# Kernel tuning notes

Measured on AMD Instinct MI355X. Metric: run time of the kernel, lower is better.

The kernel has to match this reference:

```python
import jax, jax.numpy as jnp
import numpy as np

PATCH = [2, 4, 8, 16]   # square window sizes, one per head group
LAYERS = 2
C = 128                 # channel = d_input = hidden
DK = C // len(PATCH)    # 32 channels per head group


def leaky(z):
    return jax.nn.leaky_relu(z, negative_slope=0.2)


def conv2d(x, w, b, dil=1, pad=1):
    # x: (N,C,H,W), w: (O,I,3,3)
    y = jax.lax.conv_general_dilated(
        x, w, window_strides=(1, 1), padding=((pad, pad), (pad, pad)),
        rhs_dilation=(dil, dil), dimension_numbers=('NCHW', 'OIHW', 'NCHW'))
    return y + b[None, :, None, None]


def window_attn(q, k, v, bsz, ph, pw):
    # q/k/v: (b*t, dk, h, w) -> attention over t*oh*ow patch tokens of dim dk*ph*pw
    bt, dk, h, w = q.shape
    t = bt // bsz
    oh, ow = h // ph, w // pw

    def to_tok(z):
        z = z.reshape(bsz, t, dk, oh, ph, ow, pw)
        z = z.transpose(0, 1, 3, 5, 2, 4, 6)  # (b, t, oh, ow, dk, ph, pw)
        return z.reshape(bsz, t * oh * ow, dk * ph * pw)

    qt, kt, vt = to_tok(q), to_tok(k), to_tok(v)
    scale = 1.0 / jnp.sqrt(jnp.asarray(qt.shape[-1], qt.dtype))
    scores = jnp.einsum('bld,bmd->blm', qt, kt) * scale
    p = jax.nn.softmax(scores, axis=-1)
    y = jnp.einsum('blm,bmd->bld', p, vt)
    y = y.reshape(bsz, t, oh, ow, dk, ph, pw).transpose(0, 1, 4, 2, 5, 3, 6)
    return y.reshape(bt, dk, h, w)


def transformer_block(x, Wq, bq, Wk, bk, Wv, bv, Wo, bo, Wf1, bf1, Wf2, bf2, bsz):
    # 1x1 conv embeddings as channel matmuls
    q = jnp.einsum('bihw,oi->bohw', x, Wq) + bq[None, :, None, None]
    k = jnp.einsum('bihw,oi->bohw', x, Wk) + bk[None, :, None, None]
    v = jnp.einsum('bihw,oi->bohw', x, Wv) + bv[None, :, None, None]
    outs = []
    for g, p in enumerate(PATCH):
        sl = slice(g * DK, (g + 1) * DK)
        outs.append(window_attn(q[:, sl], k[:, sl], v[:, sl], bsz, p, p))
    att = jnp.concatenate(outs, axis=1)
    x = x + leaky(conv2d(att, Wo, bo, dil=1, pad=1))
    f = leaky(conv2d(x, Wf1, bf1, dil=2, pad=2))
    f = leaky(conv2d(f, Wf2, bf2, dil=1, pad=1))
    return x + f


def setup_inputs() -> dict:
    key = jax.random.key(0)
    ks = jax.random.split(key, 14)
    g = 0.02  # init gain matching init_weights normal(0, 0.02)
    x = jax.random.normal(ks[0], (8, C, 64, 64), dtype=jnp.float32)
    mk = lambda k, shape: (g * jax.random.normal(k, shape)).astype(jnp.float32)
    return {
        'x': x,
        'Wq': mk(ks[1], (LAYERS, C, C)), 'bq': jnp.zeros((LAYERS, C), jnp.float32),
        'Wk': mk(ks[2], (LAYERS, C, C)), 'bk': jnp.zeros((LAYERS, C), jnp.float32),
        'Wv': mk(ks[3], (LAYERS, C, C)), 'bv': jnp.zeros((LAYERS, C), jnp.float32),
        'Wo': mk(ks[4], (LAYERS, C, C, 3, 3)), 'bo': jnp.zeros((LAYERS, C), jnp.float32),
        'Wf1': mk(ks[5], (LAYERS, C, C, 3, 3)), 'bf1': jnp.zeros((LAYERS, C), jnp.float32),
        'Wf2': mk(ks[6], (LAYERS, C, C, 3, 3)), 'bf2': jnp.zeros((LAYERS, C), jnp.float32),
        'bsz': 2,
    }


def reference(x, Wq, bq, Wk, bk, Wv, bv, Wo, bo, Wf1, bf1, Wf2, bf2, bsz):
    for i in range(LAYERS):
        x = transformer_block(x, Wq[i], bq[i], Wk[i], bk[i], Wv[i], bv[i],
                              Wo[i], bo[i], Wf1[i], bf1[i], Wf2[i], bf2[i], bsz)
    return x
```

## Files before the change

kernel.cpp:

```cpp
#include <hip/hip_runtime.h>

__device__ __forceinline__ unsigned short f2bf(float f) {
  union { float f; unsigned int i; } c; c.f = f;
  unsigned int i = c.i;
  i += 0x7fffu + ((i >> 16) & 1u);
  return (unsigned short)(i >> 16);
}

typedef __attribute__((ext_vector_type(8))) short bf16x8;
typedef __attribute__((ext_vector_type(4))) float f32x4;


__global__ __launch_bounds__(256) void x2hwc(const float* __restrict__ X,
                                             unsigned short* __restrict__ Xh) {
  int pixg = blockIdx.x * 256 + threadIdx.x;
  int c0 = blockIdx.y * 8;
  int bt = pixg >> 12, pix = pixg & 4095;
  const float* src = X + ((size_t)bt << 19) + (size_t)c0 * 4096 + pix;
  unsigned int pk[4];
#pragma unroll
  for (int j = 0; j < 4; j++) {
    unsigned short u0 = f2bf(src[(2 * j) * 4096]);
    unsigned short u1 = f2bf(src[(2 * j + 1) * 4096]);
    pk[j] = (unsigned int)u0 | ((unsigned int)u1 << 16);
  }
  *(uint4*)(Xh + (size_t)pixg * 128 + c0) = make_uint4(pk[0], pk[1], pk[2], pk[3]);
}

__global__ __launch_bounds__(256) void wprep3(
    const float* __restrict__ s0, const float* __restrict__ s1,
    const float* __restrict__ s2, unsigned short* __restrict__ d0,
    unsigned short* __restrict__ d1, unsigned short* __restrict__ d2) {
  int idx = blockIdx.x * 256 + threadIdx.x;
  const float* s = blockIdx.y == 0 ? s0 : (blockIdx.y == 1 ? s1 : s2);
  unsigned short* d = blockIdx.y == 0 ? d0 : (blockIdx.y == 1 ? d1 : d2);
  int j = idx & 7;
  int lane = (idx >> 3) & 63;
  int kg = lane >> 4, ml = lane & 15;
  int f = idx >> 9;
  int mf = f & 3, wm = (f >> 2) & 1, cs = (f >> 3) & 3, tap = f >> 5;
  int o = wm * 64 + mf * 16 + ml;
  int i = cs * 32 + kg * 8 + j;
  d[idx] = f2bf(s[(size_t)(o * 128 + i) * 9 + tap]);
}

__global__ __launch_bounds__(256) void wprep1(
    const float* __restrict__ s0, const float* __restrict__ s1,
    const float* __restrict__ s2, unsigned short* __restrict__ d0,
    unsigned short* __restrict__ d1, unsigned short* __restrict__ d2) {
  int idx = blockIdx.x * 256 + threadIdx.x;
  const float* s = blockIdx.y == 0 ? s0 : (blockIdx.y == 1 ? s1 : s2);
  unsigned short* d = blockIdx.y == 0 ? d0 : (blockIdx.y == 1 ? d1 : d2);
  d[idx] = f2bf(s[idx]);
}

template <int MODE>
__global__ __launch_bounds__(256) void qkv_pack(
    const unsigned short* __restrict__ Xh, const unsigned short* __restrict__ Wb,
    const float* __restrict__ Bi, unsigned short* __restrict__ P,
    unsigned short* __restrict__ VtP, unsigned short* __restrict__ Ff) {
  int tid = threadIdx.x, lane = tid & 63, wid = tid >> 6;
  int wm = wid & 1, wn = wid >> 1;
  int ml = lane & 15, kg = lane >> 4;
  int m_base = blockIdx.y * 64 + wm * 32;
  int n_base = blockIdx.x * 64 + wn * 32;
  f32x4 acc[2][2];
#pragma unroll
  for (int i = 0; i < 2; i++)
#pragma unroll
    for (int j = 0; j < 2; j++) acc[i][j] = {0.f, 0.f, 0.f, 0.f};
#pragma unroll
  for (int kc = 0; kc < 128; kc += 32) {
    bf16x8 af[2], bfr[2];
#pragma unroll
    for (int mf = 0; mf < 2; mf++)
      af[mf] = *(const bf16x8*)(Wb + (size_t)(m_base + mf * 16 + ml) * 128 + kc + kg * 8);
#pragma unroll
    for (int nf = 0; nf < 2; nf++)
      bfr[nf] = *(const bf16x8*)(Xh + (size_t)(n_base + nf * 16 + ml) * 128 + kc + kg * 8);
#pragma unroll
    for (int mf = 0; mf < 2; mf++)
#pragma unroll
      for (int nf = 0; nf < 2; nf++)
        acc[mf][nf] = __builtin_amdgcn_mfma_f32_16x16x32_bf16(af[mf], bfr[nf], acc[mf][nf], 0, 0, 0);
  }
#pragma unroll
  for (int mf = 0; mf < 2; mf++)
#pragma unroll
    for (int nf = 0; nf < 2; nf++)
#pragma unroll
      for (int r = 0; r < 4; r++) {
        int c = m_base + mf * 16 + kg * 4 + r;
        int pixg = n_base + nf * 16 + ml;
        float val = acc[mf][nf][r] + Bi[c];
        int bt = pixg >> 12, pix = pixg & 4095;
        int h = pix >> 6, w = pix & 63;
        int g = c >> 5, sh = g + 1, msk = (1 << sh) - 1, ohn = 64 >> sh;
        int b = bt >> 2, t_i = bt & 3;
        int l = (t_i * ohn + (h >> sh)) * ohn + (w >> sh);
        int Dg = 32 << (2 * sh);
        int d = ((c & 31) << (2 * sh)) + ((h & msk) << sh) + (w & msk);
        if (MODE == 0) val *= rsqrtf((float)Dg);
        unsigned short bv = f2bf(val);
        size_t bofs = (size_t)b << 19;
        if (g == 0) {
          if (MODE == 0) {
            int qt = l >> 4, mlq = l & 15, cc = d >> 5, kgq = (d >> 3) & 3, j = d & 7;
            Ff[bofs + ((size_t)(qt * 4 + cc) << 9) + (kgq * 16 + mlq) * 8 + j] = bv;
          } else if (MODE == 1) {
            int ck = l >> 6, mfk = (l >> 4) & 3, mlk = l & 15;
            int cc = d >> 5, kgk = (d >> 3) & 3, j = d & 7;
            Ff[bofs + ((size_t)(ck * 16 + cc * 4 + mfk) << 9) + (kgk * 16 + mlk) * 8 + j] = bv;
          } else {
            int ck = l >> 6, part = (l >> 5) & 1, kgv = (l >> 3) & 3, j = l & 7;
            int nf = d >> 4, mlv = d & 15;
            Ff[bofs + ((size_t)(ck * 16 + nf * 2 + part) << 9) + (kgv * 16 + mlv) * 8 + j] = bv;
          }
        } else {
          size_t base = ((size_t)g << 20) + bofs;
          if (MODE != 2) {
            P[base + (size_t)l * Dg + d] = bv;
          } else {
            int Lg = 16384 >> (2 * sh);
            VtP[base + (size_t)d * Lg + l] = bv;
          }
        }
      }
}

__global__ __launch_bounds__(256) void gemm_tn(
    const unsigned short* __restrict__ A, const unsigned short* __restrict__ B,
    float* __restrict__ C, int K, int lda, int ldb, int ldc,
    long long sA, long long sB, long long sC) {
  int tid = threadIdx.x, lane = tid & 63, wid = tid >> 6;
  int wm = wid & 1, wn = wid >> 1;
  int ml = lane & 15, kg = lane >> 4;
  A += (size_t)blockIdx.z * sA;
  B += (size_t)blockIdx.z * sB;
  C += (size_t)blockIdx.z * sC;
  int m_base = blockIdx.y * 64 + wm * 32;
  int n_base = blockIdx.x * 64 + wn * 32;
  f32x4 acc[2][2];
#pragma unroll
  for (int i = 0; i < 2; i++)
#pragma unroll
    for (int j = 0; j < 2; j++) acc[i][j] = {0.f, 0.f, 0.f, 0.f};
  for (int kc = 0; kc < K; kc += 32) {
    bf16x8 af[2], bfr[2];
#pragma unroll
    for (int mf = 0; mf < 2; mf++)
      af[mf] = *(const bf16x8*)(A + (size_t)(m_base + mf * 16 + ml) * lda + kc + kg * 8);
#pragma unroll
    for (int nf = 0; nf < 2; nf++)
      bfr[nf] = *(const bf16x8*)(B + (size_t)(n_base + nf * 16 + ml) * ldb + kc + kg * 8);
#pragma unroll
    for (int mf = 0; mf < 2; mf++)
#pragma unroll
      for (int nf = 0; nf < 2; nf++)
        acc[mf][nf] = __builtin_amdgcn_mfma_f32_16x16x32_bf16(af[mf], bfr[nf], acc[mf][nf], 0, 0, 0);
  }
#pragma unroll
  for (int mf = 0; mf < 2; mf++)
#pragma unroll
    for (int nf = 0; nf < 2; nf++)
#pragma unroll
      for (int r = 0; r < 4; r++) {
        int m = m_base + mf * 16 + kg * 4 + r;
        int n = n_base + nf * 16 + ml;
        C[(size_t)m * ldc + n] = acc[mf][nf][r];
      }
}

__global__ __launch_bounds__(256) void gemm_tn_sk(
    const unsigned short* __restrict__ A, const unsigned short* __restrict__ B,
    float* __restrict__ Cp, int lda, int ldb, int L,
    long long sA, long long sB) {
  constexpr int KC = 128;
  int tid = threadIdx.x, lane = tid & 63, wid = tid >> 6;
  int wm = wid & 1, wn = wid >> 1;
  int ml = lane & 15, kg = lane >> 4;
  int bz = blockIdx.z, b = bz & 1, split = bz >> 1;
  A += (size_t)b * sA + split * KC;
  B += (size_t)b * sB + split * KC;
  float* Ct = Cp + (size_t)bz * L * L;
  int m_base = blockIdx.y * 64 + wm * 32;
  int n_base = blockIdx.x * 64 + wn * 32;
  f32x4 acc[2][2];
#pragma unroll
  for (int i = 0; i < 2; i++)
#pragma unroll
    for (int j = 0; j < 2; j++) acc[i][j] = {0.f, 0.f, 0.f, 0.f};
#pragma unroll
  for (int kc = 0; kc < KC; kc += 32) {
    bf16x8 af[2], bfr[2];
#pragma unroll
    for (int mf = 0; mf < 2; mf++)
      af[mf] = *(const bf16x8*)(A + (size_t)(m_base + mf * 16 + ml) * lda + kc + kg * 8);
#pragma unroll
    for (int nf = 0; nf < 2; nf++)
      bfr[nf] = *(const bf16x8*)(B + (size_t)(n_base + nf * 16 + ml) * ldb + kc + kg * 8);
#pragma unroll
    for (int mf = 0; mf < 2; mf++)
#pragma unroll
      for (int nf = 0; nf < 2; nf++)
        acc[mf][nf] = __builtin_amdgcn_mfma_f32_16x16x32_bf16(af[mf], bfr[nf], acc[mf][nf], 0, 0, 0);
  }
#pragma unroll
  for (int mf = 0; mf < 2; mf++)
#pragma unroll
    for (int nf = 0; nf < 2; nf++)
#pragma unroll
      for (int r = 0; r < 4; r++) {
        int m = m_base + mf * 16 + kg * 4 + r;
        int n = n_base + nf * 16 + ml;
        Ct[(size_t)m * L + n] = acc[mf][nf][r];
      }
}

__global__ __launch_bounds__(256) void softmax_sum_bf16(
    const float* __restrict__ Sp, unsigned short* __restrict__ P, int L, int nsplit) {
  __shared__ float red[256];
  int tid = threadIdx.x;
  int b = blockIdx.x / L, m = blockIdx.x - b * L;
  const float* row = Sp + ((size_t)b * L + m) * L;
  long long pstride = 2LL * L * L;
  float val = 0.f;
  if (tid < L) {
    for (int s = 0; s < nsplit; s++) val += row[(size_t)s * pstride + tid];
  }
  red[tid] = (tid < L) ? val : -1e30f;
  __syncthreads();
  for (int s = 128; s > 0; s >>= 1) {
    if (tid < s) red[tid] = fmaxf(red[tid], red[tid + s]);
    __syncthreads();
  }
  float mx = red[0]; __syncthreads();
  float e = (tid < L) ? __expf(val - mx) : 0.f;
  red[tid] = e; __syncthreads();
  for (int s = 128; s > 0; s >>= 1) {
    if (tid < s) red[tid] += red[tid + s];
    __syncthreads();
  }
  float inv = 1.f / red[0];
  if (tid < L) P[((size_t)b * L + m) * L + tid] = f2bf(e * inv);
}

__global__ __launch_bounds__(256) void softmax_bf16(float* __restrict__ S,
                                                    unsigned short* __restrict__ P, int L) {
  __shared__ float red[256];
  int tid = threadIdx.x;
  float* p = S + (size_t)blockIdx.x * L;
  unsigned short* o = P + (size_t)blockIdx.x * L;
  float mx = -1e30f;
  for (int e = tid; e < L; e += 256) mx = fmaxf(mx, p[e]);
  red[tid] = mx; __syncthreads();
  for (int s = 128; s > 0; s >>= 1) {
    if (tid < s) red[tid] = fmaxf(red[tid], red[tid + s]);
    __syncthreads();
  }
  mx = red[0]; __syncthreads();
  float sm = 0.f;
  for (int e = tid; e < L; e += 256) {
    float v = __expf(p[e] - mx);
    p[e] = v; sm += v;
  }
  red[tid] = sm; __syncthreads();
  for (int s = 128; s > 0; s >>= 1) {
    if (tid < s) red[tid] += red[tid + s];
    __syncthreads();
  }
  float inv = 1.f / red[0];
  for (int e = tid; e < L; e += 256) o[e] = f2bf(p[e] * inv);
}

__global__ __launch_bounds__(256, 2) void flash_mfma(
    const unsigned short* __restrict__ Qf, const unsigned short* __restrict__ Kf,
    const unsigned short* __restrict__ Vf, float* __restrict__ O) {
  __shared__ float Ot[4][16][128];
  __shared__ unsigned short Pl[4][16][72];
  __shared__ float Ml[4][16], Ll[4][16];
  int tid = threadIdx.x, lane = tid & 63, wv = tid >> 6;
  int ml = lane & 15, kg = lane >> 4;
  int b = blockIdx.x >> 8, qt = blockIdx.x & 255;
  size_t bofs = (size_t)b << 19;
  int q0 = qt * 16;

  bf16x8 qf[4];
#pragma unroll
  for (int cc = 0; cc < 4; cc++)
    qf[cc] = *(const bf16x8*)(Qf + bofs + ((size_t)(qt * 4 + cc) << 9) + lane * 8);

  float m_i = -1e30f, l_i = 0.f;
  f32x4 of[8];
#pragma unroll
  for (int nf = 0; nf < 8; nf++) of[nf] = {0.f, 0.f, 0.f, 0.f};

  for (int ck = wv * 16; ck < wv * 16 + 16; ck++) {
    const unsigned short* Kc = Kf + bofs + ((size_t)ck << 13);
    const unsigned short* Vc = Vf + bofs + ((size_t)ck << 13);
    f32x4 st[4];
#pragma unroll
    for (int mf = 0; mf < 4; mf++) st[mf] = {0.f, 0.f, 0.f, 0.f};
#pragma unroll
    for (int cc = 0; cc < 4; cc++)
#pragma unroll
      for (int mf = 0; mf < 4; mf++) {
        bf16x8 kf = *(const bf16x8*)(Kc + ((cc * 4 + mf) << 9) + lane * 8);
        st[mf] = __builtin_amdgcn_mfma_f32_16x16x32_bf16(kf, qf[cc], st[mf], 0, 0, 0);
      }
    bf16x8 vf[16];
#pragma unroll
    for (int nv = 0; nv < 16; nv++)
      vf[nv] = *(const bf16x8*)(Vc + (nv << 9) + lane * 8);
    float cmax = -1e30f;
#pragma unroll
    for (int mf = 0; mf < 4; mf++)
#pragma unroll
      for (int r = 0; r < 4; r++) cmax = fmaxf(cmax, st[mf][r]);
    cmax = fmaxf(cmax, __shfl_xor(cmax, 16));
    cmax = fmaxf(cmax, __shfl_xor(cmax, 32));
    float mnew = fmaxf(m_i, cmax);
    float alpha = __expf(m_i - mnew);
    float p[4][4];
    float psum = 0.f;
#pragma unroll
    for (int mf = 0; mf < 4; mf++)
#pragma unroll
      for (int r = 0; r < 4; r++) {
        float pv = __expf(st[mf][r] - mnew);
        p[mf][r] = pv; psum += pv;
      }
    psum += __shfl_xor(psum, 16);
    psum += __shfl_xor(psum, 32);
    l_i = l_i * alpha + psum;
    m_i = mnew;
    float a0 = __shfl(alpha, kg * 4 + 0), a1 = __shfl(alpha, kg * 4 + 1);
    float a2 = __shfl(alpha, kg * 4 + 2), a3 = __shfl(alpha, kg * 4 + 3);
#pragma unroll
    for (int nf = 0; nf < 8; nf++) {
      of[nf][0] *= a0; of[nf][1] *= a1; of[nf][2] *= a2; of[nf][3] *= a3;
    }
#pragma unroll
    for (int mf = 0; mf < 4; mf++) {
      unsigned int lo = (unsigned int)f2bf(p[mf][0]) | ((unsigned int)f2bf(p[mf][1]) << 16);
      unsigned int hi = (unsigned int)f2bf(p[mf][2]) | ((unsigned int)f2bf(p[mf][3]) << 16);
      *(uint2*)&Pl[wv][ml][mf * 16 + kg * 4] = make_uint2(lo, hi);
    }
    bf16x8 pa0 = *(const bf16x8*)&Pl[wv][ml][kg * 8];
    bf16x8 pa1 = *(const bf16x8*)&Pl[wv][ml][32 + kg * 8];
#pragma unroll
    for (int nf = 0; nf < 8; nf++) {
      of[nf] = __builtin_amdgcn_mfma_f32_16x16x32_bf16(pa0, vf[nf * 2 + 0], of[nf], 0, 0, 0);
      of[nf] = __builtin_amdgcn_mfma_f32_16x16x32_bf16(pa1, vf[nf * 2 + 1], of[nf], 0, 0, 0);
    }
  }

  if (kg == 0) { Ml[wv][ml] = m_i; Ll[wv][ml] = l_i; }
  __syncthreads();
  float m0 = Ml[0][ml], m1 = Ml[1][ml], m2 = Ml[2][ml], m3 = Ml[3][ml];
  float mt = fmaxf(fmaxf(m0, m1), fmaxf(m2, m3));
  float lt = Ll[0][ml] * __expf(m0 - mt) + Ll[1][ml] * __expf(m1 - mt) +
             Ll[2][ml] * __expf(m2 - mt) + Ll[3][ml] * __expf(m3 - mt);
  float s = __expf(m_i - mt) / lt;
  float s0 = __shfl(s, kg * 4 + 0), s1 = __shfl(s, kg * 4 + 1);
  float s2 = __shfl(s, kg * 4 + 2), s3 = __shfl(s, kg * 4 + 3);
#pragma unroll
  for (int nf = 0; nf < 8; nf++) {
    Ot[wv][kg * 4 + 0][nf * 16 + ml] = of[nf][0] * s0;
    Ot[wv][kg * 4 + 1][nf * 16 + ml] = of[nf][1] * s1;
    Ot[wv][kg * 4 + 2][nf * 16 + ml] = of[nf][2] * s2;
    Ot[wv][kg * 4 + 3][nf * 16 + ml] = of[nf][3] * s3;
  }
  __syncthreads();
  int base = tid * 8;
  int q = base >> 7, d = base & 127;
  float4 r0 = make_float4(0, 0, 0, 0), r1 = make_float4(0, 0, 0, 0);
#pragma unroll
  for (int w = 0; w < 4; w++) {
    float4 a = *(const float4*)&Ot[w][q][d];
    float4 c = *(const float4*)&Ot[w][q][d + 4];
    r0.x += a.x; r0.y += a.y; r0.z += a.z; r0.w += a.w;
    r1.x += c.x; r1.y += c.y; r1.z += c.z; r1.w += c.w;
  }
  float* Op = O + bofs + (size_t)(q0 + q) * 128 + d;
  *(float4*)Op = r0;
  *(float4*)(Op + 4) = r1;
}

__global__ __launch_bounds__(256) void unpack_att_bf16(
    const float* __restrict__ opk, unsigned short* __restrict__ att) {
  int idx = blockIdx.x * 256 + threadIdx.x;
  int oct = idx & 15, pix = idx >> 4;
  int w = pix & 63, h = (pix >> 6) & 63, bt = pix >> 12;
  int c0 = oct * 8;
  int g = c0 >> 5;
  int sh = g + 1, msk = (1 << sh) - 1;
  int ohn = 64 >> sh;
  int b = bt >> 2, t_i = bt & 3;
  int l = (t_i * ohn + (h >> sh)) * ohn + (w >> sh);
  int Dg = 32 << (2 * sh);
  int dbase = ((c0 & 31) << (2 * sh)) + ((h & msk) << sh) + (w & msk);
  const float* src = opk + ((size_t)g << 20) + ((size_t)b << 19) + (size_t)l * Dg;
  int dstep = 1 << (2 * sh);
  unsigned int pk[4];
#pragma unroll
  for (int j = 0; j < 4; j++) {
    unsigned short u0 = f2bf(src[dbase + (2 * j) * dstep]);
    unsigned short u1 = f2bf(src[dbase + (2 * j + 1) * dstep]);
    pk[j] = (unsigned int)u0 | ((unsigned int)u1 << 16);
  }
  *(uint4*)(att + ((size_t)pix * 128 + c0)) = make_uint4(pk[0], pk[1], pk[2], pk[3]);
}

template <int DIL, bool WF32, bool WBF16, bool RES>
__global__ __launch_bounds__(256) void conv_mfma(
    const unsigned short* __restrict__ Xb,
    const unsigned short* __restrict__ Wt,
    const float* __restrict__ Bi,
    const float* __restrict__ Rs,
    float* __restrict__ Yf,
    unsigned short* __restrict__ Ybf) {
  __shared__ __align__(16) char Xs[3 * 17408];
  int tid = threadIdx.x;
  int lane = tid & 63, wid = tid >> 6;
  int wm = wid & 1, wn = wid >> 1;
  int ml = lane & 15, kg = lane >> 4;
  int bt = blockIdx.x >> 6, h = blockIdx.x & 63;
  const int wbase = wn * 32;

  for (int idx = tid; idx < 3264; idx += 256) {
    int row = idx / 1088, rem = idx - row * 1088;
    int pix = rem >> 4, cs = rem & 15;
    int r = h + (row - 1) * DIL;
    int w = pix - 2;
    bf16x8 v = {0, 0, 0, 0, 0, 0, 0, 0};
    if ((unsigned)r < 64u && (unsigned)w < 64u)
      v = *(const bf16x8*)(Xb + (((size_t)(bt * 64 + r) * 64 + w) << 7) + cs * 8);
    int sw = (cs & 8) | ((cs ^ (pix & 7)) & 7);
    *(bf16x8*)(&Xs[row * 17408 + pix * 256 + sw * 16]) = v;
  }
  __syncthreads();

  f32x4 acc[4][2];
#pragma unroll
  for (int i = 0; i < 4; i++)
#pragma unroll
    for (int j = 0; j < 2; j++)
      acc[i][j] = {0.f, 0.f, 0.f, 0.f};

#pragma unroll
  for (int kh = 0; kh < 3; kh++) {
#pragma unroll
    for (int kw = 0; kw < 3; kw++) {
      int shf = (kw - 1) * DIL + 2;
#pragma unroll
      for (int cs4 = 0; cs4 < 4; cs4++) {
        const unsigned short* Ap =
            Wt + ((size_t)(((kh * 3 + kw) * 4 + cs4) * 2 + wm) << 11) + lane * 8;
        bf16x8 a[4], bfr[2];
#pragma unroll
        for (int mf = 0; mf < 4; mf++)
          a[mf] = *(const bf16x8*)(Ap + (mf << 9));
#pragma unroll
        for (int nf = 0; nf < 2; nf++) {
          int px = wbase + nf * 16 + ml + shf;
          int cslot = cs4 * 4 + kg;
          int sw = (cslot & 8) | ((cslot ^ (px & 7)) & 7);
          bfr[nf] = *(const bf16x8*)(&Xs[kh * 17408 + px * 256 + sw * 16]);
        }
#pragma unroll
        for (int mf = 0; mf < 4; mf++)
#pragma unroll
          for (int nf = 0; nf < 2; nf++)
            acc[mf][nf] = __builtin_amdgcn_mfma_f32_16x16x32_bf16(
                a[mf], bfr[nf], acc[mf][nf], 0, 0, 0);
      }
    }
  }

#pragma unroll
  for (int mf = 0; mf < 4; mf++) {
    int obase = wm * 64 + mf * 16 + kg * 4;
#pragma unroll
    for (int nf = 0; nf < 2; nf++) {
      int w = wbase + nf * 16 + ml;
      float v[4];
#pragma unroll
      for (int r4 = 0; r4 < 4; r4++) {
        int o = obase + r4;
        float val = acc[mf][nf][r4] + Bi[o];
        val = val > 0.f ? val : 0.2f * val;
        size_t idx = (((size_t)bt * 128 + o) * 64 + h) * 64 + w;
        if (RES) val += Rs[idx];
        if (WF32) Yf[idx] = val;
        v[r4] = val;
      }
      if (WBF16) {
        unsigned int lo = (unsigned int)f2bf(v[0]) | ((unsigned int)f2bf(v[1]) << 16);
        unsigned int hi = (unsigned int)f2bf(v[2]) | ((unsigned int)f2bf(v[3]) << 16);
        *(uint2*)(Ybf + (((size_t)bt * 4096 + h * 64 + w) * 128 + obase)) =
            make_uint2(lo, hi);
      }
    }
  }
}

extern "C" void kernel_launch(void* const* d_in, const int* in_sizes, int n_in,
                              void* d_out, int out_size, void* d_ws, size_t ws_size,
                              hipStream_t stream) {
  (void)in_sizes; (void)n_in; (void)out_size; (void)ws_size;
  const float* x   = (const float*)d_in[0];
  const float* Wq  = (const float*)d_in[1];
  const float* bq  = (const float*)d_in[2];
  const float* Wk  = (const float*)d_in[3];
  const float* bk  = (const float*)d_in[4];
  const float* Wv  = (const float*)d_in[5];
  const float* bv  = (const float*)d_in[6];
  const float* Wo  = (const float*)d_in[7];
  const float* bo  = (const float*)d_in[8];
  const float* Wf1 = (const float*)d_in[9];
  const float* bf1 = (const float*)d_in[10];
  const float* Wf2 = (const float*)d_in[11];
  const float* bf2 = (const float*)d_in[12];
  float* out = (float*)d_out;

  char* wsb = (char*)d_ws;
  float* xcur = (float*)(wsb);
  float* opk  = (float*)(wsb + 16777216);
  float* S    = (float*)(wsb + 33554432);
  unsigned short* Qp = (unsigned short*)(wsb + 41943040);
  unsigned short* Kp = (unsigned short*)(wsb + 50331648);
  unsigned short* Vt = (unsigned short*)(wsb + 58720256);
  unsigned short* Qf = (unsigned short*)(wsb + 67108864);
  unsigned short* Kf = (unsigned short*)(wsb + 69206016);
  unsigned short* Vf = (unsigned short*)(wsb + 71303168);
  unsigned short* att_hwc  = (unsigned short*)(wsb + 73400320);
  unsigned short* xcur_hwc = (unsigned short*)(wsb + 81788928);
  unsigned short* Wt0 = (unsigned short*)(wsb + 90177536);
  unsigned short* Wt1 = (unsigned short*)(wsb + 90472448);
  unsigned short* Wt2 = (unsigned short*)(wsb + 90767360);
  unsigned short* Wqb = (unsigned short*)(wsb + 91062272);
  unsigned short* Wkb = (unsigned short*)(wsb + 91095040);
  unsigned short* Wvb = (unsigned short*)(wsb + 91127808);
  unsigned short* f1_hwc = att_hwc;
  unsigned short* Pb = xcur_hwc;

  hipMemcpyAsync(xcur, x, 16777216, hipMemcpyDeviceToDevice, stream);

  const int Ls[3] = {1024, 256, 64};
  const int Ds[3] = {512, 2048, 8192};
  dim3 blk(256);

  x2hwc<<<dim3(128, 16), blk, 0, stream>>>(x, xcur_hwc);

  for (int layer = 0; layer < 2; layer++) {
    const float* wq  = Wq  + layer * 16384;
    const float* wk  = Wk  + layer * 16384;
    const float* wv  = Wv  + layer * 16384;
    const float* bq_ = bq  + layer * 128;
    const float* bk_ = bk  + layer * 128;
    const float* bv_ = bv  + layer * 128;
    const float* wo  = Wo  + layer * 147456;
    const float* bo_ = bo  + layer * 128;
    const float* wf1 = Wf1 + layer * 147456;
    const float* bf1_ = bf1 + layer * 128;
    const float* wf2 = Wf2 + layer * 147456;
    const float* bf2_ = bf2 + layer * 128;

    wprep3<<<dim3(576, 3), blk, 0, stream>>>(wo, wf1, wf2, Wt0, Wt1, Wt2);
    wprep1<<<dim3(64, 3), blk, 0, stream>>>(wq, wk, wv, Wqb, Wkb, Wvb);

    qkv_pack<0><<<dim3(512, 2), blk, 0, stream>>>(xcur_hwc, Wqb, bq_, Qp, nullptr, Qf);
    qkv_pack<1><<<dim3(512, 2), blk, 0, stream>>>(xcur_hwc, Wkb, bk_, Kp, nullptr, Kf);
    qkv_pack<2><<<dim3(512, 2), blk, 0, stream>>>(xcur_hwc, Wvb, bv_, nullptr, Vt, Vf);

    flash_mfma<<<dim3(512), blk, 0, stream>>>(Qf, Kf, Vf, opk);

    for (int gg = 0; gg < 3; gg++) {
      int g = gg + 1;
      size_t go = (size_t)g << 20;
      int L = Ls[gg], D = Ds[gg];
      if (gg == 0) {
        gemm_tn<<<dim3(L / 64, L / 64, 2), blk, 0, stream>>>(
            Qp + go, Kp + go, S, D, D, D, L, 1LL << 19, 1LL << 19, (long long)L * L);
        softmax_bf16<<<dim3(2 * L), blk, 0, stream>>>(S, Pb, L);
      } else {
        int nsplit = D / 128;
        gemm_tn_sk<<<dim3(L / 64, L / 64, 2 * nsplit), blk, 0, stream>>>(
            Qp + go, Kp + go, S, D, D, L, 1LL << 19, 1LL << 19);
        softmax_sum_bf16<<<dim3(2 * L), blk, 0, stream>>>(S, Pb, L, nsplit);
      }
      gemm_tn<<<dim3(D / 64, L / 64, 2), blk, 0, stream>>>(
          Pb, Vt + go, opk + go, L, L, L, D, (long long)L * L, 1LL << 19, 1LL << 19);
    }

    unpack_att_bf16<<<dim3(2048), blk, 0, stream>>>(opk, att_hwc);

    conv_mfma<1, true, true, true><<<dim3(512), blk, 0, stream>>>(
        att_hwc, Wt0, bo_, xcur, xcur, xcur_hwc);
    conv_mfma<2, false, true, false><<<dim3(512), blk, 0, stream>>>(
        xcur_hwc, Wt1, bf1_, nullptr, nullptr, f1_hwc);
    if (layer == 0) {
      conv_mfma<1, true, true, true><<<dim3(512), blk, 0, stream>>>(
          f1_hwc, Wt2, bf2_, xcur, xcur, xcur_hwc);
    } else {
      conv_mfma<1, true, false, true><<<dim3(512), blk, 0, stream>>>(
          f1_hwc, Wt2, bf2_, xcur, out, nullptr);
    }
  }
}
```

Measured before the change: 630.9 us.

## Split flash attention and PV GEMMs across key halves with merge kernels

Splits the patch-2 flash attention over two key halves (doubling grid to 1024 blocks), writing unnormalized partials plus max/sum stats, then merges them in a new flash_merge kernel. Adds setprio around MFMA blocks, raises launch bounds occupancy to 3, and skips the rescale when the running max does not change. For the L=1024 and L=256 groups, the P·V GEMM is split-K in two with a sum2 reduction kernel. Intended to raise parallelism on an under-occupied grid at the cost of extra partial-buffer traffic and launches.

Result: slower. 665.3 us (+5.5%).

```diff
diff --git a/kernel.cpp b/kernel.cpp
--- a/kernel.cpp
+++ b/kernel.cpp
@@ -217,6 +217,63 @@
       }
 }
 
+__global__ __launch_bounds__(256) void gemm_tn_sk2(
+    const unsigned short* __restrict__ A, const unsigned short* __restrict__ B,
+    float* __restrict__ Cp, int KC, int lda, int ldb, int ldc,
+    long long sA, long long sB) {
+  int tid = threadIdx.x, lane = tid & 63, wid = tid >> 6;
+  int wm = wid & 1, wn = wid >> 1;
+  int ml = lane & 15, kg = lane >> 4;
+  int bz = blockIdx.z, b = bz & 1, split = bz >> 1;
+  A += (size_t)b * sA + (size_t)split * KC;
+  B += (size_t)b * sB + (size_t)split * KC;
+  size_t MN = (size_t)gridDim.y * 64 * ldc;
+  float* Ct = Cp + (size_t)bz * MN;
+  int m_base = blockIdx.y * 64 + wm * 32;
+  int n_base = blockIdx.x * 64 + wn * 32;
+  f32x4 acc[2][2];
+#pragma unroll
+  for (int i = 0; i < 2; i++)
+#pragma unroll
+    for (int j = 0; j < 2; j++) acc[i][j] = {0.f, 0.f, 0.f, 0.f};
+  for (int kc = 0; kc < KC; kc += 32) {
+    bf16x8 af[2], bfr[2];
+#pragma unroll
+    for (int mf = 0; mf < 2; mf++)
+      af[mf] = *(const bf16x8*)(A + (size_t)(m_base + mf * 16 + ml) * lda + kc + kg * 8);
+#pragma unroll
+    for (int nf = 0; nf < 2; nf++)
+      bfr[nf] = *(const bf16x8*)(B + (size_t)(n_base + nf * 16 + ml) * ldb + kc + kg * 8);
+#pragma unroll
+    for (int mf = 0; mf < 2; mf++)
+#pragma unroll
+      for (int nf = 0; nf < 2; nf++)
+        acc[mf][nf] = __builtin_amdgcn_mfma_f32_16x16x32_bf16(af[mf], bfr[nf], acc[mf][nf], 0, 0, 0);
+  }
+#pragma unroll
+  for (int mf = 0; mf < 2; mf++)
+#pragma unroll
+    for (int nf = 0; nf < 2; nf++)
+#pragma unroll
+      for (int r = 0; r < 4; r++) {
+        int m = m_base + mf * 16 + kg * 4 + r;
+        int n = n_base + nf * 16 + ml;
+        Ct[(size_t)m * ldc + n] = acc[mf][nf][r];
+      }
+}
+
+__global__ __launch_bounds__(256) void sum2(const float* __restrict__ Cp,
+                                            float* __restrict__ Out,
+                                            int MNq, long long sOut) {
+  int idx = blockIdx.x * 256 + threadIdx.x;
+  int b = idx / MNq, r = idx - b * MNq;
+  const float4* c4 = (const float4*)Cp;
+  float4 v0 = c4[(size_t)b * MNq + r];
+  float4 v1 = c4[(size_t)(2 + b) * MNq + r];
+  float4 o = make_float4(v0.x + v1.x, v0.y + v1.y, v0.z + v1.z, v0.w + v1.w);
+  ((float4*)(Out + (size_t)b * sOut))[r] = o;
+}
+
 __global__ __launch_bounds__(256) void softmax_sum_bf16(
     const float* __restrict__ Sp, unsigned short* __restrict__ P, int L, int nsplit) {
   __shared__ float red[256];
@@ -273,15 +330,17 @@
   for (int e = tid; e < L; e += 256) o[e] = f2bf(p[e] * inv);
 }
 
-__global__ __launch_bounds__(256, 2) void flash_mfma(
+__global__ __launch_bounds__(256, 3) void flash_mfma(
     const unsigned short* __restrict__ Qf, const unsigned short* __restrict__ Kf,
-    const unsigned short* __restrict__ Vf, float* __restrict__ O) {
+    const unsigned short* __restrict__ Vf, float* __restrict__ Opart,
+    float* __restrict__ MLp) {
   __shared__ float Ot[4][16][128];
   __shared__ unsigned short Pl[4][16][72];
   __shared__ float Ml[4][16], Ll[4][16];
   int tid = threadIdx.x, lane = tid & 63, wv = tid >> 6;
   int ml = lane & 15, kg = lane >> 4;
   int b = blockIdx.x >> 8, qt = blockIdx.x & 255;
+  int half = blockIdx.y;
   size_t bofs = (size_t)b << 19;
   int q0 = qt * 16;
 
@@ -295,12 +354,14 @@
 #pragma unroll
   for (int nf = 0; nf < 8; nf++) of[nf] = {0.f, 0.f, 0.f, 0.f};
 
-  for (int ck = wv * 16; ck < wv * 16 + 16; ck++) {
+  int ck0 = half * 32 + wv * 8;
+  for (int ck = ck0; ck < ck0 + 8; ck++) {
     const unsigned short* Kc = Kf + bofs + ((size_t)ck << 13);
     const unsigned short* Vc = Vf + bofs + ((size_t)ck << 13);
     f32x4 st[4];
 #pragma unroll
     for (int mf = 0; mf < 4; mf++) st[mf] = {0.f, 0.f, 0.f, 0.f};
+    __builtin_amdgcn_s_setprio(1);
 #pragma unroll
     for (int cc = 0; cc < 4; cc++)
 #pragma unroll
@@ -308,6 +369,7 @@
         bf16x8 kf = *(const bf16x8*)(Kc + ((cc * 4 + mf) << 9) + lane * 8);
         st[mf] = __builtin_amdgcn_mfma_f32_16x16x32_bf16(kf, qf[cc], st[mf], 0, 0, 0);
       }
+    __builtin_amdgcn_s_setprio(0);
     bf16x8 vf[16];
 #pragma unroll
     for (int nv = 0; nv < 16; nv++)
@@ -319,8 +381,8 @@
       for (int r = 0; r < 4; r++) cmax = fmaxf(cmax, st[mf][r]);
     cmax = fmaxf(cmax, __shfl_xor(cmax, 16));
     cmax = fmaxf(cmax, __shfl_xor(cmax, 32));
-    float mnew = fmaxf(m_i, cmax);
-    float alpha = __expf(m_i - mnew);
+    int skip = __all(cmax <= m_i);
+    float mnew = skip ? m_i : fmaxf(m_i, cmax);
     float p[4][4];
     float psum = 0.f;
 #pragma unroll
@@ -332,13 +394,18 @@
       }
     psum += __shfl_xor(psum, 16);
     psum += __shfl_xor(psum, 32);
-    l_i = l_i * alpha + psum;
-    m_i = mnew;
-    float a0 = __shfl(alpha, kg * 4 + 0), a1 = __shfl(alpha, kg * 4 + 1);
-    float a2 = __shfl(alpha, kg * 4 + 2), a3 = __shfl(alpha, kg * 4 + 3);
-#pragma unroll
-    for (int nf = 0; nf < 8; nf++) {
-      of[nf][0] *= a0; of[nf][1] *= a1; of[nf][2] *= a2; of[nf][3] *= a3;
+    if (skip) {
+      l_i += psum;
+    } else {
+      float alpha = __expf(m_i - mnew);
+      l_i = l_i * alpha + psum;
+      m_i = mnew;
+      float a0 = __shfl(alpha, kg * 4 + 0), a1 = __shfl(alpha, kg * 4 + 1);
+      float a2 = __shfl(alpha, kg * 4 + 2), a3 = __shfl(alpha, kg * 4 + 3);
+#pragma unroll
+      for (int nf = 0; nf < 8; nf++) {
+        of[nf][0] *= a0; of[nf][1] *= a1; of[nf][2] *= a2; of[nf][3] *= a3;
+      }
     }
 #pragma unroll
     for (int mf = 0; mf < 4; mf++) {
@@ -348,11 +415,13 @@
     }
     bf16x8 pa0 = *(const bf16x8*)&Pl[wv][ml][kg * 8];
     bf16x8 pa1 = *(const bf16x8*)&Pl[wv][ml][32 + kg * 8];
+    __builtin_amdgcn_s_setprio(1);
 #pragma unroll
     for (int nf = 0; nf < 8; nf++) {
       of[nf] = __builtin_amdgcn_mfma_f32_16x16x32_bf16(pa0, vf[nf * 2 + 0], of[nf], 0, 0, 0);
       of[nf] = __builtin_amdgcn_mfma_f32_16x16x32_bf16(pa1, vf[nf * 2 + 1], of[nf], 0, 0, 0);
     }
+    __builtin_amdgcn_s_setprio(0);
   }
 
   if (kg == 0) { Ml[wv][ml] = m_i; Ll[wv][ml] = l_i; }
@@ -361,7 +430,7 @@
   float mt = fmaxf(fmaxf(m0, m1), fmaxf(m2, m3));
   float lt = Ll[0][ml] * __expf(m0 - mt) + Ll[1][ml] * __expf(m1 - mt) +
              Ll[2][ml] * __expf(m2 - mt) + Ll[3][ml] * __expf(m3 - mt);
-  float s = __expf(m_i - mt) / lt;
+  float s = __expf(m_i - mt);
   float s0 = __shfl(s, kg * 4 + 0), s1 = __shfl(s, kg * 4 + 1);
   float s2 = __shfl(s, kg * 4 + 2), s3 = __shfl(s, kg * 4 + 3);
 #pragma unroll
@@ -371,6 +440,10 @@
     Ot[wv][kg * 4 + 2][nf * 16 + ml] = of[nf][2] * s2;
     Ot[wv][kg * 4 + 3][nf * 16 + ml] = of[nf][3] * s3;
   }
+  if (wv == 0 && kg == 0) {
+    MLp[half * 16384 + b * 8192 + q0 + ml] = mt;
+    MLp[half * 16384 + b * 8192 + 4096 + q0 + ml] = lt;
+  }
   __syncthreads();
   int base = tid * 8;
   int q = base >> 7, d = base & 127;
@@ -382,9 +455,28 @@
     r0.x += a.x; r0.y += a.y; r0.z += a.z; r0.w += a.w;
     r1.x += c.x; r1.y += c.y; r1.z += c.z; r1.w += c.w;
   }
-  float* Op = O + bofs + (size_t)(q0 + q) * 128 + d;
+  float* Op = Opart + ((size_t)half << 20) + bofs + (size_t)(q0 + q) * 128 + d;
   *(float4*)Op = r0;
   *(float4*)(Op + 4) = r1;
+}
+
+__global__ __launch_bounds__(256) void flash_merge(
+    const float* __restrict__ Op, const float* __restrict__ MLp,
+    float* __restrict__ O) {
+  int idx = blockIdx.x * 256 + threadIdx.x;
+  int b = idx >> 17, rem = idx & 131071;
+  int q = rem >> 5, d4 = (rem & 31) << 2;
+  float M0 = MLp[b * 8192 + q], L0 = MLp[b * 8192 + 4096 + q];
+  float M1 = MLp[16384 + b * 8192 + q], L1 = MLp[16384 + b * 8192 + 4096 + q];
+  float M = fmaxf(M0, M1);
+  float e0 = __expf(M0 - M), e1 = __expf(M1 - M);
+  float inv = 1.f / (e0 * L0 + e1 * L1);
+  size_t o0 = ((size_t)b << 19) + (size_t)q * 128 + d4;
+  float4 a = *(const float4*)(Op + o0);
+  float4 c = *(const float4*)(Op + (1 << 20) + o0);
+  float4 r = make_float4((e0 * a.x + e1 * c.x) * inv, (e0 * a.y + e1 * c.y) * inv,
+                         (e0 * a.z + e1 * c.z) * inv, (e0 * a.w + e1 * c.w) * inv);
+  *(float4*)(O + o0) = r;
 }
 
 __global__ __launch_bounds__(256) void unpack_att_bf16(
@@ -542,6 +634,7 @@
   unsigned short* Wqb = (unsigned short*)(wsb + 91062272);
   unsigned short* Wkb = (unsigned short*)(wsb + 91095040);
   unsigned short* Wvb = (unsigned short*)(wsb + 91127808);
+  float* MLp = (float*)(wsb + 91160576);
   unsigned short* f1_hwc = att_hwc;
   unsigned short* Pb = xcur_hwc;
 
@@ -574,7 +667,8 @@
     qkv_pack<1><<<dim3(512, 2), blk, 0, stream>>>(xcur_hwc, Wkb, bk_, Kp, nullptr, Kf);
     qkv_pack<2><<<dim3(512, 2), blk, 0, stream>>>(xcur_hwc, Wvb, bv_, nullptr, Vt, Vf);
 
-    flash_mfma<<<dim3(512), blk, 0, stream>>>(Qf, Kf, Vf, opk);
+    flash_mfma<<<dim3(512, 2), blk, 0, stream>>>(Qf, Kf, Vf, S, MLp);
+    flash_merge<<<dim3(1024), blk, 0, stream>>>(S, MLp, opk);
 
     for (int gg = 0; gg < 3; gg++) {
       int g = gg + 1;
@@ -590,8 +684,14 @@
             Qp + go, Kp + go, S, D, D, L, 1LL << 19, 1LL << 19);
         softmax_sum_bf16<<<dim3(2 * L), blk, 0, stream>>>(S, Pb, L, nsplit);
       }
-      gemm_tn<<<dim3(D / 64, L / 64, 2), blk, 0, stream>>>(
-          Pb, Vt + go, opk + go, L, L, L, D, (long long)L * L, 1LL << 19, 1LL << 19);
+      if (gg == 2) {
+        gemm_tn<<<dim3(D / 64, L / 64, 2), blk, 0, stream>>>(
+            Pb, Vt + go, opk + go, L, L, L, D, (long long)L * L, 1LL << 19, 1LL << 19);
+      } else {
+        gemm_tn_sk2<<<dim3(D / 64, L / 64, 4), blk, 0, stream>>>(
+            Pb, Vt + go, S, L / 2, L, L, D, (long long)L * L, 1LL << 19);
+        sum2<<<dim3(1024), blk, 0, stream>>>(S, opk + go, 131072, 1LL << 19);
+      }
     }
 
     unpack_att_bf16<<<dim3(2048), blk, 0, stream>>>(opk, att_hwc);
```
